# Optimization experiments

Measured on AMD Instinct MI355X. Metric: run time of the kernel, lower is better.

The kernel has to match this reference:

```python
import jax, jax.numpy as jnp
import numpy as np

B, N, DEG = 8, 4096, 16
E = N * DEG            # edges per graph
IN, HID, C, OUT = 128, 512, 2, 10
EPS = 1e-15


def setup_inputs() -> dict:
    key = jax.random.key(0)
    ks = jax.random.split(key, 16)
    # within-graph random edges, then offset each graph by b*N
    src = jax.random.randint(ks[0], (B, E), 0, N)
    dst = jax.random.randint(ks[1], (B, E), 0, N)
    off = (jnp.arange(B) * N)[:, None]
    edge_index = jnp.stack([(src + off).reshape(-1), (dst + off).reshape(-1)], axis=0).astype(jnp.int64)
    batch = jnp.repeat(jnp.arange(B), N).astype(jnp.int64)
    x = jax.random.normal(ks[2], (B * N, IN), dtype=jnp.float32)
    edge_weight = jax.random.uniform(ks[3], (B * E,), dtype=jnp.float32)
    g = lambda k, s: (0.02 * jax.random.normal(k, s, dtype=jnp.float32))
    return {
        "x": x, "edge_index": edge_index, "batch": batch, "edge_weight": edge_weight,
        "W_rel1": g(ks[4], (IN, HID)), "b_rel1": jnp.zeros((HID,), jnp.float32),
        "W_root1": g(ks[5], (IN, HID)),
        "W_pool": g(ks[6], (HID, C)), "b_pool": jnp.zeros((C,), jnp.float32),
        "W_rel3": g(ks[7], (HID, HID)), "b_rel3": jnp.zeros((HID,), jnp.float32),
        "W_root3": g(ks[8], (HID, HID)),
        "W_lin1": g(ks[9], (HID, HID)), "b_lin1": jnp.zeros((HID,), jnp.float32),
        "W_lin2": g(ks[10], (HID, OUT)), "b_lin2": jnp.zeros((OUT,), jnp.float32),
    }


def reference(x, edge_index, batch, edge_weight,
              W_rel1, b_rel1, W_root1, W_pool, b_pool,
              W_rel3, b_rel3, W_root3, W_lin1, b_lin1, W_lin2, b_lin2):
    src, dst = edge_index[0], edge_index[1]
    # GraphConv (aggr='add'): out = lin_rel(sum_j w_ji x_j) + lin_root(x)
    agg = jax.ops.segment_sum(x[src] * edge_weight[:, None], dst, num_segments=B * N)
    h = jax.nn.relu(agg @ W_rel1 + b_rel1 + x @ W_root1)          # [BN, HID]
    s_logits = h @ W_pool + b_pool                                 # [BN, C]

    # dense batched tensors (equal-size graphs)
    hd = h.reshape(B, N, HID)
    s = jax.nn.softmax(s_logits.reshape(B, N, C), axis=-1)
    b_idx = batch[src]
    r = src - b_idx * N
    c = dst - b_idx * N
    adj = jnp.zeros((B, N, N), jnp.float32).at[b_idx, r, c].add(edge_weight)

    # dense mincut pooling
    out = jnp.einsum('bnc,bnf->bcf', s, hd)                        # [B, C, HID]
    sA = jnp.einsum('bnc,bnm->bcm', s, adj)
    out_adj = jnp.einsum('bcm,bmk->bck', sA, s)                    # [B, C, C]
    mincut_num = jnp.einsum('bcc->b', out_adj)
    d = adj.sum(-1)                                                # [B, N]
    mincut_den = jnp.einsum('bnc,bn,bnc->b', s, d, s)
    mc_loss = jnp.mean(-(mincut_num / mincut_den))
    ss = jnp.einsum('bnc,bnk->bck', s, s)
    ss_n = ss / jnp.linalg.norm(ss, axis=(1, 2), keepdims=True)
    i_s = jnp.eye(C, dtype=jnp.float32) / jnp.sqrt(jnp.float32(C))
    o_loss = jnp.mean(jnp.linalg.norm(ss_n - i_s[None], axis=(1, 2)))
    # zero diagonal + symmetric degree normalization
    out_adj = out_adj * (1.0 - jnp.eye(C, dtype=jnp.float32))[None]
    d2 = jnp.sqrt(out_adj.sum(-1)) + EPS                           # [B, C]
    out_adj = out_adj / d2[:, :, None] / d2[:, None, :]

    # conv3 on pooled graph: edges (row->col) of dense adj => agg = A^T x
    agg3 = jnp.einsum('bij,bif->bjf', out_adj, out)
    x3 = agg3 @ W_rel3 + b_rel3 + out @ W_root3                    # [B, C, HID]
    xm = x3.mean(axis=1)                                           # [B, HID]
    h2 = jax.nn.relu(xm @ W_lin1 + b_lin1)
    logits = h2 @ W_lin2 + b_lin2
    return (jax.nn.log_softmax(logits, axis=-1), mc_loss, o_loss, s_logits, out_adj)
```

## Files before the change

kernel.cpp:

```cpp
#include <hip/hip_runtime.h>
#include <hip/hip_bf16.h>

#define BB 8
#define NN 4096
#define EE 65536
#define BE (BB*EE)
#define BN (BB*NN)
#define INF 128
#define HID 512
#define CC 2
#define OUTC 10
#define ELLCAP 64

typedef __bf16 bf16x8_t __attribute__((ext_vector_type(8)));
typedef float  f32x4_t  __attribute__((ext_vector_type(4)));

__device__ __forceinline__ ushort f2bf(float f) {
  union { float f; unsigned u; } v; v.f = f;
  unsigned r = v.u + 0x7FFFu + ((v.u >> 16) & 1u);
  return (ushort)(r >> 16);
}
__device__ __forceinline__ float bf2f(ushort s) {
  union { unsigned u; float f; } v; v.u = ((unsigned)s) << 16;
  return v.f;
}

__global__ __launch_bounds__(256) void front(
    const int* __restrict__ src, const int* __restrict__ dst,
    const float* __restrict__ ew, const float* __restrict__ x,
    const float* __restrict__ Wrel, const float* __restrict__ Wroot,
    int* __restrict__ deg, int2* __restrict__ ell,
    ushort* __restrict__ Ab, ushort* __restrict__ Bb) {
  int blk = blockIdx.x;
  int tid = threadIdx.x;
  if (blk < 4096) {
    int g = blk * 256 + tid;
    float4 v = *(const float4*)&x[(size_t)g * 4];
    int m = g >> 5;
    int kin = (g & 31) * 4;
    ushort4 o;
    o.x = f2bf(v.x); o.y = f2bf(v.y); o.z = f2bf(v.z); o.w = f2bf(v.w);
    *(ushort4*)&Ab[(size_t)m * 256 + 128 + kin] = o;
  } else if (blk < 6144) {
    int e = (blk - 4096) * 256 + tid;
    int d = dst[e];
    int p = atomicAdd(&deg[d], 1);
    if (p < ELLCAP) {
      int2 v; v.x = src[e]; v.y = __float_as_int(ew[e]);
      ell[(size_t)d * ELLCAP + p] = v;
    }
  } else {
    int g = (blk - 6144) * 256 + tid;
    int n = g & 511, k = g >> 9;
    float w = (k < 128) ? Wrel[k * 512 + n] : Wroot[(k - 128) * 512 + n];
    Bb[n * 256 + k] = f2bf(w);
  }
}

__global__ __launch_bounds__(256) void gather_ell(
    const int* __restrict__ deg, const int2* __restrict__ ell,
    ushort* __restrict__ Ab) {
  int n = blockIdx.x * 4 + (threadIdx.x >> 6);
  int lane = threadIdx.x & 63;
  int d = deg[n]; if (d > ELLCAP) d = ELLCAP;
  const int2* ep = ell + (size_t)n * ELLCAP;
  float ax = 0.f, ay = 0.f;
  int j = 0;
  for (; j + 3 < d; j += 4) {
    int2 v0 = ep[j], v1 = ep[j + 1], v2 = ep[j + 2], v3 = ep[j + 3];
    ushort2 u0 = *(const ushort2*)&Ab[(size_t)v0.x * 256 + 128 + lane * 2];
    ushort2 u1 = *(const ushort2*)&Ab[(size_t)v1.x * 256 + 128 + lane * 2];
    ushort2 u2 = *(const ushort2*)&Ab[(size_t)v2.x * 256 + 128 + lane * 2];
    ushort2 u3 = *(const ushort2*)&Ab[(size_t)v3.x * 256 + 128 + lane * 2];
    float w0 = __int_as_float(v0.y), w1 = __int_as_float(v1.y);
    float w2 = __int_as_float(v2.y), w3 = __int_as_float(v3.y);
    ax += w0 * bf2f(u0.x) + w1 * bf2f(u1.x) + w2 * bf2f(u2.x) + w3 * bf2f(u3.x);
    ay += w0 * bf2f(u0.y) + w1 * bf2f(u1.y) + w2 * bf2f(u2.y) + w3 * bf2f(u3.y);
  }
  for (; j < d; ++j) {
    int2 v0 = ep[j];
    float w0 = __int_as_float(v0.y);
    ushort2 u0 = *(const ushort2*)&Ab[(size_t)v0.x * 256 + 128 + lane * 2];
    ax += w0 * bf2f(u0.x);
    ay += w0 * bf2f(u0.y);
  }
  ushort2 o; o.x = f2bf(ax); o.y = f2bf(ay);
  *(ushort2*)&Ab[(size_t)n * 256 + lane * 2] = o;
}

#define CPAD 72
__global__ __launch_bounds__(256) void gemm_mfma(
    const ushort* __restrict__ Ab, const ushort* __restrict__ Bb,
    const float* __restrict__ brel, ushort* __restrict__ hw) {
  __shared__ ushort As[64 * 256];
  __shared__ ushort Bs[64 * 256];
  int tid = threadIdx.x;
  int blk = blockIdx.x;
  int xcd = blk & 7;
  int idx = blk >> 3;
  int by = xcd * 64 + (idx & 63);
  int bx = idx >> 6;
  int m0 = by * 64, n0 = bx * 64;

#pragma unroll
  for (int i = 0; i < 8; ++i) {
    int g = tid + i * 256;
    int r = g >> 5, c = g & 31;
    int cs = c ^ (r & 31);
    *(uint4*)&As[(r * 32 + cs) * 8] = *(const uint4*)&Ab[(size_t)(m0 + r) * 256 + c * 8];
    *(uint4*)&Bs[(r * 32 + cs) * 8] = *(const uint4*)&Bb[(size_t)(n0 + r) * 256 + c * 8];
  }
  __syncthreads();

  int wave = tid >> 6, lane = tid & 63;
  int wm = (wave >> 1) * 32, wn = (wave & 1) * 32;
  int l16 = lane & 15, quad = lane >> 4;

  f32x4_t acc[2][2];
#pragma unroll
  for (int f = 0; f < 2; ++f)
#pragma unroll
    for (int g = 0; g < 2; ++g) acc[f][g] = (f32x4_t){0.f, 0.f, 0.f, 0.f};

  int arow[2] = {wm + l16, wm + 16 + l16};
  int brow[2] = {wn + l16, wn + 16 + l16};

#pragma unroll
  for (int kc = 0; kc < 8; ++kc) {
    int cl = kc * 4 + quad;
    bf16x8_t af[2], bf[2];
#pragma unroll
    for (int f = 0; f < 2; ++f) {
      af[f] = *(const bf16x8_t*)&As[(arow[f] * 32 + (cl ^ (arow[f] & 31))) * 8];
      bf[f] = *(const bf16x8_t*)&Bs[(brow[f] * 32 + (cl ^ (brow[f] & 31))) * 8];
    }
#pragma unroll
    for (int f = 0; f < 2; ++f)
#pragma unroll
      for (int g = 0; g < 2; ++g)
        acc[f][g] = __builtin_amdgcn_mfma_f32_16x16x32_bf16(af[f], bf[g], acc[f][g], 0, 0, 0);
  }
  __syncthreads();

  ushort* Cs = As;
#pragma unroll
  for (int g = 0; g < 2; ++g) {
    int col = wn + g * 16 + l16;
    float bias = brel[n0 + col];
#pragma unroll
    for (int f = 0; f < 2; ++f) {
      int rowb = wm + f * 16 + quad * 4;
#pragma unroll
      for (int r = 0; r < 4; ++r) {
        float v = fmaxf(acc[f][g][r] + bias, 0.f);
        Cs[(rowb + r) * CPAD + col] = f2bf(v);
      }
    }
  }
  __syncthreads();
  {
    int r = tid >> 2, co = (tid & 3) * 16;
    uint4 v0 = *(uint4*)&Cs[r * CPAD + co];
    uint4 v1 = *(uint4*)&Cs[r * CPAD + co + 8];
    *(uint4*)&hw[(size_t)(m0 + r) * 512 + n0 + co] = v0;
    *(uint4*)&hw[(size_t)(m0 + r) * 512 + n0 + co + 8] = v1;
  }
}

__global__ __launch_bounds__(256) void pool_node(
    const ushort* __restrict__ hw, const float* __restrict__ Wp,
    const float* __restrict__ bp, float* __restrict__ s,
    float* __restrict__ slog, float* __restrict__ outpart,
    float* __restrict__ ssacc) {
  __shared__ float red[4][1024];
  __shared__ float ssr[4][3];
  int blk = blockIdx.x;
  int b = blk >> 6;
  int wave = threadIdx.x >> 6, lane = threadIdx.x & 63;
  int n0 = blk * 64 + wave * 16;
  int f0 = lane * 8;

  float wp0[8], wp1[8];
#pragma unroll
  for (int j = 0; j < 8; ++j) {
    wp0[j] = Wp[(f0 + j) * 2];
    wp1[j] = Wp[(f0 + j) * 2 + 1];
  }
  float bp0 = bp[0], bp1 = bp[1];
  float o0[8] = {0, 0, 0, 0, 0, 0, 0, 0};
  float o1[8] = {0, 0, 0, 0, 0, 0, 0, 0};
  float sa = 0.f, sb = 0.f, sc2 = 0.f;

  for (int i = 0; i < 16; ++i) {
    int n = n0 + i;
    bf16x8_t hv = *(const bf16x8_t*)&hw[(size_t)n * HID + f0];
    const ushort* hp = (const ushort*)&hv;
    float h[8];
    float a0 = 0.f, a1 = 0.f;
#pragma unroll
    for (int j = 0; j < 8; ++j) {
      h[j] = bf2f(hp[j]);
      a0 += h[j] * wp0[j];
      a1 += h[j] * wp1[j];
    }
#pragma unroll
    for (int off = 32; off; off >>= 1) {
      a0 += __shfl_down(a0, off, 64);
      a1 += __shfl_down(a1, off, 64);
    }
    float s0 = 0.f, s1 = 0.f;
    if (lane == 0) {
      float l0 = a0 + bp0, l1 = a1 + bp1;
      slog[n * 2] = l0;
      slog[n * 2 + 1] = l1;
      float m = fmaxf(l0, l1);
      float e0 = expf(l0 - m), e1 = expf(l1 - m);
      float inv = 1.f / (e0 + e1);
      s0 = e0 * inv; s1 = e1 * inv;
      s[n * 2] = s0;
      s[n * 2 + 1] = s1;
      sa += s0 * s0; sb += s0 * s1; sc2 += s1 * s1;
    }
    s0 = __shfl(s0, 0, 64);
    s1 = __shfl(s1, 0, 64);
#pragma unroll
    for (int j = 0; j < 8; ++j) {
      o0[j] += s0 * h[j];
      o1[j] += s1 * h[j];
    }
  }

#pragma unroll
  for (int j = 0; j < 8; ++j) {
    red[wave][f0 + j] = o0[j];
    red[wave][512 + f0 + j] = o1[j];
  }
  if (lane == 0) { ssr[wave][0] = sa; ssr[wave][1] = sb; ssr[wave][2] = sc2; }
  __syncthreads();
  int t = threadIdx.x;
#pragma unroll
  for (int q = 0; q < 4; ++q) {
    int idx = t + q * 256;
    float v = red[0][idx] + red[1][idx] + red[2][idx] + red[3][idx];
    outpart[(size_t)blk * 1024 + idx] = v;
  }
  if (t < 3) {
    float v = ssr[0][t] + ssr[1][t] + ssr[2][t] + ssr[3][t];
    atomicAdd(&ssacc[b * 4 + t], v);
  }
}

__global__ __launch_bounds__(256) void edge_pass2(
    const int* __restrict__ src, const int* __restrict__ dst,
    const float* __restrict__ ew, const float* __restrict__ s,
    float* __restrict__ oadj, float* __restrict__ mden) {
  int b = blockIdx.x >> 6;
  int sub = blockIdx.x & 63;
  int base = b * EE + sub * 1024;
  float p00 = 0, p01 = 0, p10 = 0, p11 = 0, md = 0;
  for (int i = threadIdx.x; i < 1024; i += 256) {
    int e = base + i;
    int r = src[e], c = dst[e];
    float w = ew[e];
    float s0r = s[r * 2], s1r = s[r * 2 + 1];
    float s0c = s[c * 2], s1c = s[c * 2 + 1];
    p00 += w * s0r * s0c; p01 += w * s0r * s1c;
    p10 += w * s1r * s0c; p11 += w * s1r * s1c;
    md  += w * (s0r * s0r + s1r * s1r);
  }
#pragma unroll
  for (int off = 32; off; off >>= 1) {
    p00 += __shfl_down(p00, off, 64);
    p01 += __shfl_down(p01, off, 64);
    p10 += __shfl_down(p10, off, 64);
    p11 += __shfl_down(p11, off, 64);
    md  += __shfl_down(md,  off, 64);
  }
  __shared__ float red[4][5];
  int wave = threadIdx.x >> 6, lane = threadIdx.x & 63;
  if (lane == 0) {
    red[wave][0] = p00; red[wave][1] = p01;
    red[wave][2] = p10; red[wave][3] = p11;
    red[wave][4] = md;
  }
  __syncthreads();
  if (threadIdx.x < 4) {
    float v = red[0][threadIdx.x] + red[1][threadIdx.x] +
              red[2][threadIdx.x] + red[3][threadIdx.x];
    atomicAdd(&oadj[b * 4 + threadIdx.x], v);
  } else if (threadIdx.x == 4) {
    float v = red[0][4] + red[1][4] + red[2][4] + red[3][4];
    atomicAdd(&mden[b], v);
  }
}

__global__ __launch_bounds__(256) void finalize_a(
    const float* __restrict__ outpart, const float* __restrict__ oadj,
    const float* __restrict__ ssacc, const float* __restrict__ mden,
    float* __restrict__ uv, float* __restrict__ dout) {
  __shared__ float sc[2];
  int b = blockIdx.x, t = threadIdx.x;
  if (t == 0) {
    float r00 = oadj[b * 4 + 0], r01 = oadj[b * 4 + 1];
    float r10 = oadj[b * 4 + 2], r11 = oadj[b * 4 + 3];
    atomicAdd(&dout[80], -((r00 + r11) / mden[b]) / (float)BB);
    float a = ssacc[b * 4 + 0], bb = ssacc[b * 4 + 1], c = ssacc[b * 4 + 2];
    float nrm = sqrtf(a * a + 2.f * bb * bb + c * c);
    float q = 0.70710678118654752f;
    float da = a / nrm - q, db = bb / nrm, dc = c / nrm - q;
    atomicAdd(&dout[81], sqrtf(da * da + 2.f * db * db + dc * dc) / (float)BB);
    float d20 = sqrtf(r01) + 1e-15f;
    float d21 = sqrtf(r10) + 1e-15f;
    float oa01 = r01 / (d20 * d21);
    float oa10 = r10 / (d21 * d20);
    dout[65618 + b * 4 + 0] = 0.f;
    dout[65618 + b * 4 + 1] = oa01;
    dout[65618 + b * 4 + 2] = oa10;
    dout[65618 + b * 4 + 3] = 0.f;
    sc[0] = oa01; sc[1] = oa10;
  }
  __syncthreads();
  float oa01 = sc[0], oa10 = sc[1];
  for (int f = t; f < HID; f += 256) {
    float o0 = 0.f, o1 = 0.f;
    for (int i = 0; i < 64; ++i) {
      o0 += outpart[(size_t)(b * 64 + i) * 1024 + f];
      o1 += outpart[(size_t)(b * 64 + i) * 1024 + 512 + f];
    }
    uv[b * HID + f] = oa10 * o1 + oa01 * o0;
    uv[BB * HID + b * HID + f] = o0 + o1;
  }
}

__global__ __launch_bounds__(256) void conv3_part(
    const float* __restrict__ uv, const float* __restrict__ Wrel3,
    const float* __restrict__ Wroot3, float* __restrict__ xmacc) {
  __shared__ float us[8][32], vs[8][32];
  __shared__ float red[4][64][8];
  int blk = blockIdx.x;
  int fc = blk & 7, kc = blk >> 3;
  int t = threadIdx.x;
  {
    int b = t >> 5, k = t & 31;
    us[b][k] = uv[b * HID + kc * 32 + k];
    vs[b][k] = uv[BB * HID + b * HID + kc * 32 + k];
  }
  __syncthreads();
  int f = fc * 64 + (t & 63);
  int ks = t >> 6;
  float acc[8] = {0, 0, 0, 0, 0, 0, 0, 0};
#pragma unroll
  for (int j = 0; j < 8; ++j) {
    int kl = ks * 8 + j;
    int k = kc * 32 + kl;
    float wr = Wrel3[k * HID + f];
    float wo = Wroot3[k * HID + f];
#pragma unroll
    for (int b = 0; b < 8; ++b)
      acc[b] += us[b][kl] * wr + vs[b][kl] * wo;
  }
#pragma unroll
  for (int b = 0; b < 8; ++b) red[ks][t & 63][b] = acc[b];
  __syncthreads();
  if (ks == 0) {
    int fl = t & 63;
#pragma unroll
    for (int b = 0; b < 8; ++b) {
      float v = red[0][fl][b] + red[1][fl][b] + red[2][fl][b] + red[3][fl][b];
      atomicAdd(&xmacc[b * HID + f], v);
    }
  }
}

__global__ __launch_bounds__(256) void lin1_part(
    const float* __restrict__ xmacc, const float* __restrict__ brel3,
    const float* __restrict__ Wlin1, float* __restrict__ h2acc) {
  __shared__ float xs[8][32];
  __shared__ float red[4][64][8];
  int blk = blockIdx.x;
  int fc = blk & 7, kc = blk >> 3;
  int t = threadIdx.x;
  {
    int b = t >> 5, k = t & 31;
    xs[b][k] = 0.5f * xmacc[b * HID + kc * 32 + k] + brel3[kc * 32 + k];
  }
  __syncthreads();
  int f = fc * 64 + (t & 63);
  int ks = t >> 6;
  float acc[8] = {0, 0, 0, 0, 0, 0, 0, 0};
#pragma unroll
  for (int j = 0; j < 8; ++j) {
    int kl = ks * 8 + j;
    int k = kc * 32 + kl;
    float w = Wlin1[k * HID + f];
#pragma unroll
    for (int b = 0; b < 8; ++b)
      acc[b] += xs[b][kl] * w;
  }
#pragma unroll
  for (int b = 0; b < 8; ++b) red[ks][t & 63][b] = acc[b];
  __syncthreads();
  if (ks == 0) {
    int fl = t & 63;
#pragma unroll
    for (int b = 0; b < 8; ++b) {
      float v = red[0][fl][b] + red[1][fl][b] + red[2][fl][b] + red[3][fl][b];
      atomicAdd(&h2acc[b * HID + f], v);
    }
  }
}

__global__ __launch_bounds__(256) void head(
    const float* __restrict__ h2acc, const float* __restrict__ blin1,
    const float* __restrict__ Wlin2, const float* __restrict__ blin2,
    float* __restrict__ dout) {
  __shared__ float hs[HID];
  __shared__ float lg[16];
  __shared__ float lse;
  int b = blockIdx.x, t = threadIdx.x;
  for (int i = t; i < HID; i += 256)
    hs[i] = fmaxf(h2acc[b * HID + i] + blin1[i], 0.f);
  __syncthreads();
  int wave = t >> 6, lane = t & 63;
  for (int o = wave; o < OUTC; o += 4) {
    float acc = 0.f;
    for (int k = lane; k < HID; k += 64)
      acc += hs[k] * Wlin2[k * OUTC + o];
#pragma unroll
    for (int off = 32; off; off >>= 1) acc += __shfl_down(acc, off, 64);
    if (lane == 0) lg[o] = acc + blin2[o];
  }
  __syncthreads();
  if (t == 0) {
    float m = lg[0];
    for (int o = 1; o < OUTC; ++o) m = fmaxf(m, lg[o]);
    float se = 0.f;
    for (int o = 0; o < OUTC; ++o) se += expf(lg[o] - m);
    lse = m + logf(se);
  }
  __syncthreads();
  if (t < OUTC) dout[b * OUTC + t] = lg[t] - lse;
}

extern "C" void kernel_launch(void* const* d_in, const int* in_sizes, int n_in,
                              void* d_out, int out_size, void* d_ws, size_t ws_size,
                              hipStream_t stream) {
  const float* x      = (const float*)d_in[0];
  const int*   ei     = (const int*)d_in[1];
  const float* ew     = (const float*)d_in[3];
  const float* Wrel1  = (const float*)d_in[4];
  const float* brel1  = (const float*)d_in[5];
  const float* Wroot1 = (const float*)d_in[6];
  const float* Wpool  = (const float*)d_in[7];
  const float* bpool  = (const float*)d_in[8];
  const float* Wrel3  = (const float*)d_in[9];
  const float* brel3  = (const float*)d_in[10];
  const float* Wroot3 = (const float*)d_in[11];
  const float* Wlin1  = (const float*)d_in[12];
  const float* blin1  = (const float*)d_in[13];
  const float* Wlin2  = (const float*)d_in[14];
  const float* blin2  = (const float*)d_in[15];
  float* out = (float*)d_out;
  float* ws  = (float*)d_ws;

  float* oadj  = ws + 40960;
  float* ssacc = oadj + 32;
  float* mden  = ssacc + 32;
  int*   deg   = (int*)(mden + 8);
  float* xmacc = ws + 73800;
  float* h2acc = xmacc + 4096;
  ushort* Ab   = (ushort*)(ws + 106568);
  ushort* Bb   = (ushort*)(ws + 4300872);
  ushort* hbf  = (ushort*)(ws + 4366408);
  float* outpart = ws + 12763208;
  int2*  ell   = (int2*)(ws + 4366408);
  float* s     = ws + 106568;
  float* uv    = (float*)deg;

  const int* src = ei;
  const int* dst = ei + BE;

  hipMemsetAsync(ws + 40960, 0, (size_t)41032 * sizeof(float), stream);
  hipMemsetAsync(out + 80, 0, 2 * sizeof(float), stream);

  front      <<<6656, 256, 0, stream>>>(src, dst, ew, x, Wrel1, Wroot1,
                                        deg, ell, Ab, Bb);
  gather_ell <<<BN / 4, 256, 0, stream>>>(deg, ell, Ab);
  gemm_mfma  <<<4096, 256, 0, stream>>>(Ab, Bb, brel1, hbf);
  pool_node  <<<512, 256, 0, stream>>>(hbf, Wpool, bpool, s, out + 82, outpart, ssacc);
  edge_pass2 <<<BB * 64, 256, 0, stream>>>(src, dst, ew, s, oadj, mden);
  finalize_a <<<BB, 256, 0, stream>>>(outpart, oadj, ssacc, mden, uv, out);
  conv3_part <<<128, 256, 0, stream>>>(uv, Wrel3, Wroot3, xmacc);
  lin1_part  <<<128, 256, 0, stream>>>(xmacc, brel3, Wlin1, h2acc);
  head       <<<BB, 256, 0, stream>>>(h2acc, blin1, Wlin2, blin2, out);
}
```

Before: 232.7 us.

## Fuse post-GEMM tail kernels into one cooperative kernel with grid syncs

Replaces the six tail launches (pool_node, edge_pass2, finalize_a, conv3_part, lin1_part, head) with a single cooperative kernel whose stages are separated by grid.sync. The aim is to remove per-launch overhead and the idle gaps between small, low-occupancy kernels. finalize_a is also spread over 64 blocks instead of 8. The xmacc/h2acc accumulators are now zeroed inside the kernel rather than by the memset. The cost is several grid-wide barriers, and the requirement that all 512 blocks be co-resident.

```diff
diff --git a/kernel.cpp b/kernel.cpp
--- a/kernel.cpp
+++ b/kernel.cpp
@@ -1,5 +1,8 @@
 #include <hip/hip_runtime.h>
 #include <hip/hip_bf16.h>
+#include <hip/hip_cooperative_groups.h>
+
+namespace cg = cooperative_groups;
 
 #define BB 8
 #define NN 4096
@@ -167,279 +170,293 @@
   }
 }
 
-__global__ __launch_bounds__(256) void pool_node(
+__global__ __launch_bounds__(256) void tail_coop(
+    const int* __restrict__ src, const int* __restrict__ dst,
+    const float* __restrict__ ew,
     const ushort* __restrict__ hw, const float* __restrict__ Wp,
-    const float* __restrict__ bp, float* __restrict__ s,
-    float* __restrict__ slog, float* __restrict__ outpart,
-    float* __restrict__ ssacc) {
-  __shared__ float red[4][1024];
-  __shared__ float ssr[4][3];
-  int blk = blockIdx.x;
-  int b = blk >> 6;
-  int wave = threadIdx.x >> 6, lane = threadIdx.x & 63;
-  int n0 = blk * 64 + wave * 16;
-  int f0 = lane * 8;
-
-  float wp0[8], wp1[8];
-#pragma unroll
-  for (int j = 0; j < 8; ++j) {
-    wp0[j] = Wp[(f0 + j) * 2];
-    wp1[j] = Wp[(f0 + j) * 2 + 1];
-  }
-  float bp0 = bp[0], bp1 = bp[1];
-  float o0[8] = {0, 0, 0, 0, 0, 0, 0, 0};
-  float o1[8] = {0, 0, 0, 0, 0, 0, 0, 0};
-  float sa = 0.f, sb = 0.f, sc2 = 0.f;
-
-  for (int i = 0; i < 16; ++i) {
-    int n = n0 + i;
-    bf16x8_t hv = *(const bf16x8_t*)&hw[(size_t)n * HID + f0];
-    const ushort* hp = (const ushort*)&hv;
-    float h[8];
-    float a0 = 0.f, a1 = 0.f;
-#pragma unroll
-    for (int j = 0; j < 8; ++j) {
-      h[j] = bf2f(hp[j]);
-      a0 += h[j] * wp0[j];
-      a1 += h[j] * wp1[j];
-    }
-#pragma unroll
-    for (int off = 32; off; off >>= 1) {
-      a0 += __shfl_down(a0, off, 64);
-      a1 += __shfl_down(a1, off, 64);
-    }
-    float s0 = 0.f, s1 = 0.f;
-    if (lane == 0) {
-      float l0 = a0 + bp0, l1 = a1 + bp1;
-      slog[n * 2] = l0;
-      slog[n * 2 + 1] = l1;
-      float m = fmaxf(l0, l1);
-      float e0 = expf(l0 - m), e1 = expf(l1 - m);
-      float inv = 1.f / (e0 + e1);
-      s0 = e0 * inv; s1 = e1 * inv;
-      s[n * 2] = s0;
-      s[n * 2 + 1] = s1;
-      sa += s0 * s0; sb += s0 * s1; sc2 += s1 * s1;
-    }
-    s0 = __shfl(s0, 0, 64);
-    s1 = __shfl(s1, 0, 64);
-#pragma unroll
-    for (int j = 0; j < 8; ++j) {
-      o0[j] += s0 * h[j];
-      o1[j] += s1 * h[j];
-    }
-  }
-
-#pragma unroll
-  for (int j = 0; j < 8; ++j) {
-    red[wave][f0 + j] = o0[j];
-    red[wave][512 + f0 + j] = o1[j];
-  }
-  if (lane == 0) { ssr[wave][0] = sa; ssr[wave][1] = sb; ssr[wave][2] = sc2; }
-  __syncthreads();
-  int t = threadIdx.x;
-#pragma unroll
-  for (int q = 0; q < 4; ++q) {
-    int idx = t + q * 256;
-    float v = red[0][idx] + red[1][idx] + red[2][idx] + red[3][idx];
-    outpart[(size_t)blk * 1024 + idx] = v;
-  }
-  if (t < 3) {
-    float v = ssr[0][t] + ssr[1][t] + ssr[2][t] + ssr[3][t];
-    atomicAdd(&ssacc[b * 4 + t], v);
-  }
-}
-
-__global__ __launch_bounds__(256) void edge_pass2(
-    const int* __restrict__ src, const int* __restrict__ dst,
-    const float* __restrict__ ew, const float* __restrict__ s,
-    float* __restrict__ oadj, float* __restrict__ mden) {
-  int b = blockIdx.x >> 6;
-  int sub = blockIdx.x & 63;
-  int base = b * EE + sub * 1024;
-  float p00 = 0, p01 = 0, p10 = 0, p11 = 0, md = 0;
-  for (int i = threadIdx.x; i < 1024; i += 256) {
-    int e = base + i;
-    int r = src[e], c = dst[e];
-    float w = ew[e];
-    float s0r = s[r * 2], s1r = s[r * 2 + 1];
-    float s0c = s[c * 2], s1c = s[c * 2 + 1];
-    p00 += w * s0r * s0c; p01 += w * s0r * s1c;
-    p10 += w * s1r * s0c; p11 += w * s1r * s1c;
-    md  += w * (s0r * s0r + s1r * s1r);
-  }
-#pragma unroll
-  for (int off = 32; off; off >>= 1) {
-    p00 += __shfl_down(p00, off, 64);
-    p01 += __shfl_down(p01, off, 64);
-    p10 += __shfl_down(p10, off, 64);
-    p11 += __shfl_down(p11, off, 64);
-    md  += __shfl_down(md,  off, 64);
-  }
-  __shared__ float red[4][5];
-  int wave = threadIdx.x >> 6, lane = threadIdx.x & 63;
-  if (lane == 0) {
-    red[wave][0] = p00; red[wave][1] = p01;
-    red[wave][2] = p10; red[wave][3] = p11;
-    red[wave][4] = md;
-  }
-  __syncthreads();
-  if (threadIdx.x < 4) {
-    float v = red[0][threadIdx.x] + red[1][threadIdx.x] +
-              red[2][threadIdx.x] + red[3][threadIdx.x];
-    atomicAdd(&oadj[b * 4 + threadIdx.x], v);
-  } else if (threadIdx.x == 4) {
-    float v = red[0][4] + red[1][4] + red[2][4] + red[3][4];
-    atomicAdd(&mden[b], v);
-  }
-}
-
-__global__ __launch_bounds__(256) void finalize_a(
-    const float* __restrict__ outpart, const float* __restrict__ oadj,
-    const float* __restrict__ ssacc, const float* __restrict__ mden,
-    float* __restrict__ uv, float* __restrict__ dout) {
-  __shared__ float sc[2];
-  int b = blockIdx.x, t = threadIdx.x;
-  if (t == 0) {
-    float r00 = oadj[b * 4 + 0], r01 = oadj[b * 4 + 1];
-    float r10 = oadj[b * 4 + 2], r11 = oadj[b * 4 + 3];
-    atomicAdd(&dout[80], -((r00 + r11) / mden[b]) / (float)BB);
-    float a = ssacc[b * 4 + 0], bb = ssacc[b * 4 + 1], c = ssacc[b * 4 + 2];
-    float nrm = sqrtf(a * a + 2.f * bb * bb + c * c);
-    float q = 0.70710678118654752f;
-    float da = a / nrm - q, db = bb / nrm, dc = c / nrm - q;
-    atomicAdd(&dout[81], sqrtf(da * da + 2.f * db * db + dc * dc) / (float)BB);
-    float d20 = sqrtf(r01) + 1e-15f;
-    float d21 = sqrtf(r10) + 1e-15f;
-    float oa01 = r01 / (d20 * d21);
-    float oa10 = r10 / (d21 * d20);
-    dout[65618 + b * 4 + 0] = 0.f;
-    dout[65618 + b * 4 + 1] = oa01;
-    dout[65618 + b * 4 + 2] = oa10;
-    dout[65618 + b * 4 + 3] = 0.f;
-    sc[0] = oa01; sc[1] = oa10;
-  }
-  __syncthreads();
-  float oa01 = sc[0], oa10 = sc[1];
-  for (int f = t; f < HID; f += 256) {
-    float o0 = 0.f, o1 = 0.f;
-    for (int i = 0; i < 64; ++i) {
-      o0 += outpart[(size_t)(b * 64 + i) * 1024 + f];
-      o1 += outpart[(size_t)(b * 64 + i) * 1024 + 512 + f];
-    }
-    uv[b * HID + f] = oa10 * o1 + oa01 * o0;
-    uv[BB * HID + b * HID + f] = o0 + o1;
-  }
-}
-
-__global__ __launch_bounds__(256) void conv3_part(
-    const float* __restrict__ uv, const float* __restrict__ Wrel3,
-    const float* __restrict__ Wroot3, float* __restrict__ xmacc) {
-  __shared__ float us[8][32], vs[8][32];
-  __shared__ float red[4][64][8];
-  int blk = blockIdx.x;
-  int fc = blk & 7, kc = blk >> 3;
-  int t = threadIdx.x;
-  {
-    int b = t >> 5, k = t & 31;
-    us[b][k] = uv[b * HID + kc * 32 + k];
-    vs[b][k] = uv[BB * HID + b * HID + kc * 32 + k];
-  }
-  __syncthreads();
-  int f = fc * 64 + (t & 63);
-  int ks = t >> 6;
-  float acc[8] = {0, 0, 0, 0, 0, 0, 0, 0};
-#pragma unroll
-  for (int j = 0; j < 8; ++j) {
-    int kl = ks * 8 + j;
-    int k = kc * 32 + kl;
-    float wr = Wrel3[k * HID + f];
-    float wo = Wroot3[k * HID + f];
-#pragma unroll
-    for (int b = 0; b < 8; ++b)
-      acc[b] += us[b][kl] * wr + vs[b][kl] * wo;
-  }
-#pragma unroll
-  for (int b = 0; b < 8; ++b) red[ks][t & 63][b] = acc[b];
-  __syncthreads();
-  if (ks == 0) {
-    int fl = t & 63;
-#pragma unroll
-    for (int b = 0; b < 8; ++b) {
-      float v = red[0][fl][b] + red[1][fl][b] + red[2][fl][b] + red[3][fl][b];
-      atomicAdd(&xmacc[b * HID + f], v);
-    }
-  }
-}
-
-__global__ __launch_bounds__(256) void lin1_part(
-    const float* __restrict__ xmacc, const float* __restrict__ brel3,
-    const float* __restrict__ Wlin1, float* __restrict__ h2acc) {
-  __shared__ float xs[8][32];
-  __shared__ float red[4][64][8];
-  int blk = blockIdx.x;
-  int fc = blk & 7, kc = blk >> 3;
-  int t = threadIdx.x;
-  {
-    int b = t >> 5, k = t & 31;
-    xs[b][k] = 0.5f * xmacc[b * HID + kc * 32 + k] + brel3[kc * 32 + k];
-  }
-  __syncthreads();
-  int f = fc * 64 + (t & 63);
-  int ks = t >> 6;
-  float acc[8] = {0, 0, 0, 0, 0, 0, 0, 0};
-#pragma unroll
-  for (int j = 0; j < 8; ++j) {
-    int kl = ks * 8 + j;
-    int k = kc * 32 + kl;
-    float w = Wlin1[k * HID + f];
-#pragma unroll
-    for (int b = 0; b < 8; ++b)
-      acc[b] += xs[b][kl] * w;
-  }
-#pragma unroll
-  for (int b = 0; b < 8; ++b) red[ks][t & 63][b] = acc[b];
-  __syncthreads();
-  if (ks == 0) {
-    int fl = t & 63;
-#pragma unroll
-    for (int b = 0; b < 8; ++b) {
-      float v = red[0][fl][b] + red[1][fl][b] + red[2][fl][b] + red[3][fl][b];
-      atomicAdd(&h2acc[b * HID + f], v);
-    }
-  }
-}
-
-__global__ __launch_bounds__(256) void head(
-    const float* __restrict__ h2acc, const float* __restrict__ blin1,
+    const float* __restrict__ bp,
+    float* __restrict__ s, float* __restrict__ slog,
+    float* __restrict__ outpart, float* __restrict__ ssacc,
+    float* __restrict__ oadj, float* __restrict__ mden,
+    float* __restrict__ uv, float* __restrict__ xmacc, float* __restrict__ h2acc,
+    const float* __restrict__ Wrel3, const float* __restrict__ Wroot3,
+    const float* __restrict__ brel3,
+    const float* __restrict__ Wlin1, const float* __restrict__ blin1,
     const float* __restrict__ Wlin2, const float* __restrict__ blin2,
     float* __restrict__ dout) {
-  __shared__ float hs[HID];
+  cg::grid_group grid = cg::this_grid();
+  __shared__ float smem[4][1024];
+  __shared__ float ssr[4][3];
+  __shared__ float er[4][5];
+  __shared__ float uvs[2][8][32];
+  __shared__ float sc2[2];
   __shared__ float lg[16];
-  __shared__ float lse;
-  int b = blockIdx.x, t = threadIdx.x;
-  for (int i = t; i < HID; i += 256)
-    hs[i] = fmaxf(h2acc[b * HID + i] + blin1[i], 0.f);
-  __syncthreads();
-  int wave = t >> 6, lane = t & 63;
-  for (int o = wave; o < OUTC; o += 4) {
-    float acc = 0.f;
-    for (int k = lane; k < HID; k += 64)
-      acc += hs[k] * Wlin2[k * OUTC + o];
-#pragma unroll
-    for (int off = 32; off; off >>= 1) acc += __shfl_down(acc, off, 64);
-    if (lane == 0) lg[o] = acc + blin2[o];
-  }
-  __syncthreads();
-  if (t == 0) {
-    float m = lg[0];
-    for (int o = 1; o < OUTC; ++o) m = fmaxf(m, lg[o]);
-    float se = 0.f;
-    for (int o = 0; o < OUTC; ++o) se += expf(lg[o] - m);
-    lse = m + logf(se);
-  }
-  __syncthreads();
-  if (t < OUTC) dout[b * OUTC + t] = lg[t] - lse;
+  __shared__ float lsev;
+
+  int tid = threadIdx.x;
+  int wave = tid >> 6, lane = tid & 63;
+  int f0 = lane * 8;
+
+  {
+    float wp0[8], wp1[8];
+#pragma unroll
+    for (int j = 0; j < 8; ++j) {
+      wp0[j] = Wp[(f0 + j) * 2];
+      wp1[j] = Wp[(f0 + j) * 2 + 1];
+    }
+    float bp0 = bp[0], bp1 = bp[1];
+
+    for (int blk = blockIdx.x; blk < 512; blk += gridDim.x) {
+      int b = blk >> 6;
+      int n0 = blk * 64 + wave * 16;
+      float o0[8] = {0, 0, 0, 0, 0, 0, 0, 0};
+      float o1[8] = {0, 0, 0, 0, 0, 0, 0, 0};
+      float sa = 0.f, sb = 0.f, sq = 0.f;
+      for (int i = 0; i < 16; ++i) {
+        int n = n0 + i;
+        bf16x8_t hv = *(const bf16x8_t*)&hw[(size_t)n * HID + f0];
+        const ushort* hp = (const ushort*)&hv;
+        float h[8];
+        float a0 = 0.f, a1 = 0.f;
+#pragma unroll
+        for (int j = 0; j < 8; ++j) {
+          h[j] = bf2f(hp[j]);
+          a0 += h[j] * wp0[j];
+          a1 += h[j] * wp1[j];
+        }
+#pragma unroll
+        for (int off = 32; off; off >>= 1) {
+          a0 += __shfl_down(a0, off, 64);
+          a1 += __shfl_down(a1, off, 64);
+        }
+        float s0 = 0.f, s1 = 0.f;
+        if (lane == 0) {
+          float l0 = a0 + bp0, l1 = a1 + bp1;
+          slog[n * 2] = l0;
+          slog[n * 2 + 1] = l1;
+          float m = fmaxf(l0, l1);
+          float e0 = expf(l0 - m), e1 = expf(l1 - m);
+          float inv = 1.f / (e0 + e1);
+          s0 = e0 * inv; s1 = e1 * inv;
+          s[n * 2] = s0;
+          s[n * 2 + 1] = s1;
+          sa += s0 * s0; sb += s0 * s1; sq += s1 * s1;
+        }
+        s0 = __shfl(s0, 0, 64);
+        s1 = __shfl(s1, 0, 64);
+#pragma unroll
+        for (int j = 0; j < 8; ++j) {
+          o0[j] += s0 * h[j];
+          o1[j] += s1 * h[j];
+        }
+      }
+#pragma unroll
+      for (int j = 0; j < 8; ++j) {
+        smem[wave][f0 + j] = o0[j];
+        smem[wave][512 + f0 + j] = o1[j];
+      }
+      if (lane == 0) { ssr[wave][0] = sa; ssr[wave][1] = sb; ssr[wave][2] = sq; }
+      __syncthreads();
+#pragma unroll
+      for (int q = 0; q < 4; ++q) {
+        int idx = tid + q * 256;
+        float v = smem[0][idx] + smem[1][idx] + smem[2][idx] + smem[3][idx];
+        outpart[(size_t)blk * 1024 + idx] = v;
+      }
+      if (tid < 3) {
+        float v = ssr[0][tid] + ssr[1][tid] + ssr[2][tid] + ssr[3][tid];
+        atomicAdd(&ssacc[b * 4 + tid], v);
+      }
+      __syncthreads();
+    }
+  }
+  if (tid < 16) xmacc[blockIdx.x * 16 + tid] = 0.f;
+  grid.sync();
+
+  for (int vb = blockIdx.x; vb < 512; vb += gridDim.x) {
+    int b = vb >> 6;
+    int sub = vb & 63;
+    int base = b * EE + sub * 1024;
+    float p00 = 0, p01 = 0, p10 = 0, p11 = 0, md = 0;
+    for (int i = tid; i < 1024; i += 256) {
+      int e = base + i;
+      int r = src[e], c = dst[e];
+      float w = ew[e];
+      float s0r = s[r * 2], s1r = s[r * 2 + 1];
+      float s0c = s[c * 2], s1c = s[c * 2 + 1];
+      p00 += w * s0r * s0c; p01 += w * s0r * s1c;
+      p10 += w * s1r * s0c; p11 += w * s1r * s1c;
+      md  += w * (s0r * s0r + s1r * s1r);
+    }
+#pragma unroll
+    for (int off = 32; off; off >>= 1) {
+      p00 += __shfl_down(p00, off, 64);
+      p01 += __shfl_down(p01, off, 64);
+      p10 += __shfl_down(p10, off, 64);
+      p11 += __shfl_down(p11, off, 64);
+      md  += __shfl_down(md,  off, 64);
+    }
+    if (lane == 0) {
+      er[wave][0] = p00; er[wave][1] = p01;
+      er[wave][2] = p10; er[wave][3] = p11;
+      er[wave][4] = md;
+    }
+    __syncthreads();
+    if (tid < 4) {
+      float v = er[0][tid] + er[1][tid] + er[2][tid] + er[3][tid];
+      atomicAdd(&oadj[b * 4 + tid], v);
+    } else if (tid == 4) {
+      float v = er[0][4] + er[1][4] + er[2][4] + er[3][4];
+      atomicAdd(&mden[b], v);
+    }
+    __syncthreads();
+  }
+  grid.sync();
+
+  if (blockIdx.x < 64) {
+    int b = blockIdx.x >> 3, fc = blockIdx.x & 7;
+    if (tid == 0) {
+      float r00 = oadj[b * 4 + 0], r01 = oadj[b * 4 + 1];
+      float r10 = oadj[b * 4 + 2], r11 = oadj[b * 4 + 3];
+      float d20 = sqrtf(r01) + 1e-15f;
+      float d21 = sqrtf(r10) + 1e-15f;
+      float oa01 = r01 / (d20 * d21);
+      float oa10 = r10 / (d21 * d20);
+      sc2[0] = oa01; sc2[1] = oa10;
+      if (fc == 0) {
+        atomicAdd(&dout[80], -((r00 + r11) / mden[b]) / (float)BB);
+        float a = ssacc[b * 4 + 0], bb = ssacc[b * 4 + 1], c = ssacc[b * 4 + 2];
+        float nrm = sqrtf(a * a + 2.f * bb * bb + c * c);
+        float q = 0.70710678118654752f;
+        float da = a / nrm - q, db = bb / nrm, dc = c / nrm - q;
+        atomicAdd(&dout[81], sqrtf(da * da + 2.f * db * db + dc * dc) / (float)BB);
+        dout[65618 + b * 4 + 0] = 0.f;
+        dout[65618 + b * 4 + 1] = oa01;
+        dout[65618 + b * 4 + 2] = oa10;
+        dout[65618 + b * 4 + 3] = 0.f;
+      }
+    }
+    __syncthreads();
+    float oa01 = sc2[0], oa10 = sc2[1];
+    int f = fc * 64 + (tid & 63);
+    int ic = tid >> 6;
+    float o0s = 0.f, o1s = 0.f;
+    for (int i = ic * 16; i < ic * 16 + 16; ++i) {
+      o0s += outpart[(size_t)(b * 64 + i) * 1024 + f];
+      o1s += outpart[(size_t)(b * 64 + i) * 1024 + 512 + f];
+    }
+    float* r0 = &smem[0][0];
+    float* r1 = &smem[1][0];
+    r0[ic * 64 + (tid & 63)] = o0s;
+    r1[ic * 64 + (tid & 63)] = o1s;
+    __syncthreads();
+    if (ic == 0) {
+      int fl = tid & 63;
+      float a0 = r0[fl] + r0[64 + fl] + r0[128 + fl] + r0[192 + fl];
+      float a1 = r1[fl] + r1[64 + fl] + r1[128 + fl] + r1[192 + fl];
+      uv[b * HID + f] = oa10 * a1 + oa01 * a0;
+      uv[BB * HID + b * HID + f] = a0 + a1;
+    }
+  }
+  grid.sync();
+
+  if (blockIdx.x < 128) {
+    int fc = blockIdx.x & 7, kc = blockIdx.x >> 3;
+    {
+      int b = tid >> 5, k = tid & 31;
+      uvs[0][b][k] = uv[b * HID + kc * 32 + k];
+      uvs[1][b][k] = uv[BB * HID + b * HID + kc * 32 + k];
+    }
+    __syncthreads();
+    int f = fc * 64 + (tid & 63);
+    int ks = tid >> 6;
+    float acc[8] = {0, 0, 0, 0, 0, 0, 0, 0};
+#pragma unroll
+    for (int j = 0; j < 8; ++j) {
+      int kl = ks * 8 + j;
+      int k = kc * 32 + kl;
+      float wr = Wrel3[k * HID + f];
+      float wo = Wroot3[k * HID + f];
+#pragma unroll
+      for (int b = 0; b < 8; ++b)
+        acc[b] += uvs[0][b][kl] * wr + uvs[1][b][kl] * wo;
+    }
+    float* redf = &smem[0][0];
+#pragma unroll
+    for (int b = 0; b < 8; ++b) redf[(ks * 64 + (tid & 63)) * 8 + b] = acc[b];
+    __syncthreads();
+    if (ks == 0) {
+      int fl = tid & 63;
+#pragma unroll
+      for (int b = 0; b < 8; ++b) {
+        float v = redf[(0 * 64 + fl) * 8 + b] + redf[(1 * 64 + fl) * 8 + b] +
+                  redf[(2 * 64 + fl) * 8 + b] + redf[(3 * 64 + fl) * 8 + b];
+        atomicAdd(&xmacc[b * HID + f], v);
+      }
+    }
+  }
+  grid.sync();
+
+  if (blockIdx.x < 128) {
+    int fc = blockIdx.x & 7, kc = blockIdx.x >> 3;
+    {
+      int b = tid >> 5, k = tid & 31;
+      uvs[0][b][k] = 0.5f * xmacc[b * HID + kc * 32 + k] + brel3[kc * 32 + k];
+    }
+    __syncthreads();
+    int f = fc * 64 + (tid & 63);
+    int ks = tid >> 6;
+    float acc[8] = {0, 0, 0, 0, 0, 0, 0, 0};
+#pragma unroll
+    for (int j = 0; j < 8; ++j) {
+      int kl = ks * 8 + j;
+      int k = kc * 32 + kl;
+      float w = Wlin1[k * HID + f];
+#pragma unroll
+      for (int b = 0; b < 8; ++b)
+        acc[b] += uvs[0][b][kl] * w;
+    }
+    float* redf = &smem[0][0];
+#pragma unroll
+    for (int b = 0; b < 8; ++b) redf[(ks * 64 + (tid & 63)) * 8 + b] = acc[b];
+    __syncthreads();
+    if (ks == 0) {
+      int fl = tid & 63;
+#pragma unroll
+      for (int b = 0; b < 8; ++b) {
+        float v = redf[(0 * 64 + fl) * 8 + b] + redf[(1 * 64 + fl) * 8 + b] +
+                  redf[(2 * 64 + fl) * 8 + b] + redf[(3 * 64 + fl) * 8 + b];
+        atomicAdd(&h2acc[b * HID + f], v);
+      }
+    }
+  }
+  grid.sync();
+
+  if (blockIdx.x < 8) {
+    int b = blockIdx.x;
+    float* hs = &smem[0][0];
+    for (int i = tid; i < HID; i += 256)
+      hs[i] = fmaxf(h2acc[b * HID + i] + blin1[i], 0.f);
+    __syncthreads();
+    for (int o = wave; o < OUTC; o += 4) {
+      float acc = 0.f;
+      for (int k = lane; k < HID; k += 64)
+        acc += hs[k] * Wlin2[k * OUTC + o];
+#pragma unroll
+      for (int off = 32; off; off >>= 1) acc += __shfl_down(acc, off, 64);
+      if (lane == 0) lg[o] = acc + blin2[o];
+    }
+    __syncthreads();
+    if (tid == 0) {
+      float m = lg[0];
+      for (int o = 1; o < OUTC; ++o) m = fmaxf(m, lg[o]);
+      float se = 0.f;
+      for (int o = 0; o < OUTC; ++o) se += expf(lg[o] - m);
+      lsev = m + logf(se);
+    }
+    __syncthreads();
+    if (tid < OUTC) dout[b * OUTC + tid] = lg[tid] - lsev;
+  }
 }
 
 extern "C" void kernel_launch(void* const* d_in, const int* in_sizes, int n_in,
@@ -479,18 +496,25 @@
 
   const int* src = ei;
   const int* dst = ei + BE;
-
-  hipMemsetAsync(ws + 40960, 0, (size_t)41032 * sizeof(float), stream);
+  float* slogp = out + 82;
+
+  hipMemsetAsync(ws + 40960, 0, (size_t)32840 * sizeof(float), stream);
   hipMemsetAsync(out + 80, 0, 2 * sizeof(float), stream);
 
   front      <<<6656, 256, 0, stream>>>(src, dst, ew, x, Wrel1, Wroot1,
                                         deg, ell, Ab, Bb);
   gather_ell <<<BN / 4, 256, 0, stream>>>(deg, ell, Ab);
   gemm_mfma  <<<4096, 256, 0, stream>>>(Ab, Bb, brel1, hbf);
-  pool_node  <<<512, 256, 0, stream>>>(hbf, Wpool, bpool, s, out + 82, outpart, ssacc);
-  edge_pass2 <<<BB * 64, 256, 0, stream>>>(src, dst, ew, s, oadj, mden);
-  finalize_a <<<BB, 256, 0, stream>>>(outpart, oadj, ssacc, mden, uv, out);
-  conv3_part <<<128, 256, 0, stream>>>(uv, Wrel3, Wroot3, xmacc);
-  lin1_part  <<<128, 256, 0, stream>>>(xmacc, brel3, Wlin1, h2acc);
-  head       <<<BB, 256, 0, stream>>>(h2acc, blin1, Wlin2, blin2, out);
-}
+
+  void* targs[] = {
+    (void*)&src, (void*)&dst, (void*)&ew,
+    (void*)&hbf, (void*)&Wpool, (void*)&bpool,
+    (void*)&s, (void*)&slogp, (void*)&outpart, (void*)&ssacc,
+    (void*)&oadj, (void*)&mden, (void*)&uv, (void*)&xmacc, (void*)&h2acc,
+    (void*)&Wrel3, (void*)&Wroot3, (void*)&brel3,
+    (void*)&Wlin1, (void*)&blin1, (void*)&Wlin2, (void*)&blin2,
+    (void*)&out
+  };
+  hipLaunchCooperativeKernel((void*)tail_coop, dim3(512), dim3(256),
+                             targs, 0, stream);
+}
```

New measurement: 494.1 us. 2.12x slower.
